# Kernel tuning notes

Measured on AMD Instinct MI355X. Metric: run time of the kernel, lower is better.

## Reference

```python
import jax, jax.numpy as jnp
import numpy as np

B, H, S, D = 2, 16, 2048, 64

def setup_inputs() -> dict:
    key = jax.random.key(0)
    kq, kk, kv = jax.random.split(key, 3)
    Q = jax.random.normal(kq, (B, H, S, D), dtype=jnp.float32)
    K = jax.random.normal(kk, (B, H, S, D), dtype=jnp.float32)
    V = jax.random.normal(kv, (B, H, S, D), dtype=jnp.float32)
    # causal mask, broadcastable over batch and heads
    mask = jnp.tril(jnp.ones((S, S), dtype=bool))[None, None, :, :]
    return {"Q": Q, "K": K, "V": V, "mask": mask}

def reference(Q, K, V, mask):
    # scores: [B,H,S,S]
    scores = jnp.einsum('bhqd,bhkd->bhqk', Q, K)
    # original applies mask (-inf) BEFORE scaling; -inf/scale == -inf so math matches
    scores = jnp.where(mask, scores, -jnp.inf)
    scores = scores / jnp.sqrt(jnp.float32(K.shape[-1]))
    attn = jax.nn.softmax(scores, axis=-1)
    return jnp.einsum('bhqk,bhkd->bhqd', attn, V)
```

## Files before the change

### kernel.cpp

```cpp
#include <hip/hip_runtime.h>

#define SEQ 2048
#define HD  64
#define SCALE 0.18033688011111772f

typedef __bf16 bf16x8 __attribute__((ext_vector_type(8)));
typedef __bf16 bf16x4 __attribute__((ext_vector_type(4)));
typedef float  f32x4  __attribute__((ext_vector_type(4)));
typedef float  f32x16 __attribute__((ext_vector_type(16)));

#define BAR_LGKM() asm volatile("s_waitcnt lgkmcnt(0)\n\ts_barrier" ::: "memory")

__global__ __launch_bounds__(256, 4) void attn_fwd(
    const float* __restrict__ Q,
    const float* __restrict__ K,
    const float* __restrict__ V,
    float* __restrict__ O)
{
    __shared__ __align__(16) unsigned char smem[26624];
    #define KBp(kh,key,c8) ((__bf16*)(smem +         (((kh)<<12) + ((key)<<7) + ((c8)<<4))))
    #define VTp(kh,r,c8)   ((__bf16*)(smem +  8192 + (((kh)<<12) + ((r)<<6)   + ((c8)<<4))))
    #define PWp(w,n,koff)  ((__bf16*)(smem + 16384 + ((w)*2560 + (n)*80 + ((koff)<<1))))

    const int tid   = threadIdx.x;
    const int wave  = tid >> 6;
    const int lane  = tid & 63;
    const int n     = lane & 31;
    const int p     = lane >> 5;
    const int strip = wave & 1;
    const int kh    = wave >> 1;

    const int x  = blockIdx.x;
    const int bh = x & 31;
    const int s  = x >> 5;
    const int q  = (s & 16) ? (31 - (s & 15)) : s;

    const int q0    = q * 64 + strip * 32;
    const int iters = q + 1;
    const int tS0   = kh * (q + 1);

    const float* __restrict__ Qh = Q + (size_t)bh * SEQ * HD;
    const float* __restrict__ Kh = K + (size_t)bh * SEQ * HD;
    const float* __restrict__ Vh = V + (size_t)bh * SEQ * HD;
    float* __restrict__       Oh = O + (size_t)bh * SEQ * HD;

    bf16x8 qf[4];
    {
        const float* qrow = Qh + (size_t)(q0 + n) * HD;
        #pragma unroll
        for (int c = 0; c < 4; ++c) {
            f32x4 a = *(const f32x4*)(qrow + 16 * c + 8 * p);
            f32x4 b = *(const f32x4*)(qrow + 16 * c + 8 * p + 4);
            #pragma unroll
            for (int j = 0; j < 4; ++j) {
                qf[c][j]     = (__bf16)(a[j] * SCALE);
                qf[c][4 + j] = (__bf16)(b[j] * SCALE);
            }
        }
    }

    f32x16 oT[2] = {};
    float  l_own = 0.f;

    const int local = tid & 127;
    const int key_s = local >> 2;
    const int dgi   = local & 3;
    const int Ls    = local & 31;
    const int ko    = local >> 5;
    const int swk   = key_s & 7;
    const int swv   = Ls & 3;

    const float* kbase = Kh + (size_t)key_s * HD + dgi * 16;
    const float* vbase = Vh + (size_t)(ko * 8) * HD + 2 * Ls;

    f32x4  kst[4];
    float2 vst[8];
    {
        const float* kp = kbase + (size_t)(32 * tS0) * HD;
        #pragma unroll
        for (int i = 0; i < 4; ++i) kst[i] = *(const f32x4*)(kp + 4 * i);
        const float* vp = vbase + (size_t)(32 * tS0) * HD;
        #pragma unroll
        for (int i = 0; i < 8; ++i) vst[i] = *(const float2*)(vp + (size_t)i * HD);
    }

    for (int i = 0; i < iters; ++i) {
        BAR_LGKM();

        {
            bf16x8 w0, w1;
            #pragma unroll
            for (int j = 0; j < 4; ++j) {
                w0[j] = (__bf16)kst[0][j]; w0[4 + j] = (__bf16)kst[1][j];
                w1[j] = (__bf16)kst[2][j]; w1[4 + j] = (__bf16)kst[3][j];
            }
            *(bf16x8*)KBp(kh, key_s, (2 * dgi)     ^ swk) = w0;
            *(bf16x8*)KBp(kh, key_s, (2 * dgi + 1) ^ swk) = w1;

            bf16x8 v0, v1;
            #pragma unroll
            for (int j = 0; j < 8; ++j) { v0[j] = (__bf16)vst[j].x; v1[j] = (__bf16)vst[j].y; }
            *(bf16x8*)VTp(kh, 2 * Ls,     ko ^ swv) = v0;
            *(bf16x8*)VTp(kh, 2 * Ls + 1, ko ^ swv) = v1;
        }

        if (i + 1 < iters) {
            const size_t off = (size_t)(32 * (tS0 + i + 1)) * HD;
            const float* kp = kbase + off;
            #pragma unroll
            for (int j = 0; j < 4; ++j) kst[j] = *(const f32x4*)(kp + 4 * j);
            const float* vp = vbase + off;
            #pragma unroll
            for (int j = 0; j < 8; ++j) vst[j] = *(const float2*)(vp + (size_t)j * HD);
        }

        BAR_LGKM();

        if (!kh || (i < q + strip)) {
            f32x16 sT = {};
            #pragma unroll
            for (int cc = 0; cc < 4; ++cc) {
                bf16x8 kf = *(const bf16x8*)KBp(kh, n, (2 * cc + p) ^ (n & 7));
                sT = __builtin_amdgcn_mfma_f32_32x32x16_bf16(kf, qf[cc], sT, 0, 0, 0);
            }

            const int  T    = tS0 + i;
            const bool diag = (T == 2 * q + strip);

            float pv[16];
            float ts = 0.f;
            #pragma unroll
            for (int r = 0; r < 16; ++r) {
                float pe = __builtin_amdgcn_exp2f(sT[r]);
                if (diag) {
                    const int kk = (r & 3) + 8 * (r >> 2) + 4 * p;
                    pe = (kk <= n) ? pe : 0.f;
                }
                pv[r] = pe;
                ts += pe;
            }
            l_own += ts;

            #pragma unroll
            for (int m = 0; m < 4; ++m) {
                bf16x4 pk;
                #pragma unroll
                for (int j = 0; j < 4; ++j) pk[j] = (__bf16)pv[4 * m + j];
                *(bf16x4*)PWp(wave, n, 8 * m + 4 * p) = pk;
            }
            bf16x8 pf0 = *(const bf16x8*)PWp(wave, n, 8 * p);
            bf16x8 pf1 = *(const bf16x8*)PWp(wave, n, 16 + 8 * p);

            const int swn = (n >> 1) & 3;
            #pragma unroll
            for (int dg = 0; dg < 2; ++dg) {
                bf16x8 vf0 = *(const bf16x8*)VTp(kh, 32 * dg + n, p ^ swn);
                bf16x8 vf1 = *(const bf16x8*)VTp(kh, 32 * dg + n, (2 + p) ^ swn);
                oT[dg] = __builtin_amdgcn_mfma_f32_32x32x16_bf16(vf0, pf0, oT[dg], 0, 0, 0);
                oT[dg] = __builtin_amdgcn_mfma_f32_32x32x16_bf16(vf1, pf1, oT[dg], 0, 0, 0);
            }
        }
    }

    __syncthreads();
    float* Os = (float*)smem;
    const int cb = strip * 2112;
    float l_part = l_own + __shfl_xor(l_own, 32, 64);

    if (kh == 1) {
        #pragma unroll
        for (int dg = 0; dg < 2; ++dg)
            #pragma unroll
            for (int r = 0; r < 16; ++r)
                Os[cb + (dg * 16 + r) * 64 + lane] = oT[dg][r];
        Os[cb + 2048 + lane] = l_part;
    }
    __syncthreads();
    if (kh == 0) {
        const float linv = 1.0f / (l_part + Os[cb + 2048 + lane]);
        #pragma unroll
        for (int dg = 0; dg < 2; ++dg) {
            #pragma unroll
            for (int u = 0; u < 4; ++u) {
                f32x4 o;
                #pragma unroll
                for (int j = 0; j < 4; ++j) {
                    const int r = 4 * u + j;
                    o[j] = (oT[dg][r] + Os[cb + (dg * 16 + r) * 64 + lane]) * linv;
                }
                *(f32x4*)&Oh[(size_t)(q0 + n) * HD + dg * 32 + u * 8 + 4 * p] = o;
            }
        }
    }
}

extern "C" void kernel_launch(void* const* d_in, const int* in_sizes, int n_in,
                              void* d_out, int out_size, void* d_ws, size_t ws_size,
                              hipStream_t stream) {
    const float* Q = (const float*)d_in[0];
    const float* K = (const float*)d_in[1];
    const float* V = (const float*)d_in[2];
    float* O = (float*)d_out;

    dim3 grid(1024);
    dim3 block(256);
    attn_fwd<<<grid, block, 0, stream>>>(Q, K, V, O);
}
```

Measured before the change: 136.4 us.

## Double-buffer K/V tiles, swap P via permlane32 instead of LDS, add setprio

K/V shared-memory tiles are now double-buffered, so each iteration needs one barrier instead of two. The next tile is staged into the alternate buffer after compute, and global loads run two tiles ahead. The P matrix transpose through shared memory is replaced by bf16 packing plus v_permlane32_swap register exchanges. s_setprio raises wave priority around the MFMA section. This cuts barrier and LDS round-trip costs, but grows LDS to 32KB and extends register live ranges.

```diff
diff --git a/kernel.cpp b/kernel.cpp
--- a/kernel.cpp
+++ b/kernel.cpp
@@ -5,11 +5,29 @@
 #define SCALE 0.18033688011111772f
 
 typedef __bf16 bf16x8 __attribute__((ext_vector_type(8)));
-typedef __bf16 bf16x4 __attribute__((ext_vector_type(4)));
+typedef __bf16 bf16x2 __attribute__((ext_vector_type(2)));
 typedef float  f32x4  __attribute__((ext_vector_type(4)));
 typedef float  f32x16 __attribute__((ext_vector_type(16)));
 
 #define BAR_LGKM() asm volatile("s_waitcnt lgkmcnt(0)\n\ts_barrier" ::: "memory")
+
+union PU { unsigned u[4]; bf16x8 v; };
+
+__device__ __forceinline__ unsigned pk2(float lo, float hi) {
+    union { unsigned u; bf16x2 v; } t;
+    t.v = bf16x2{(__bf16)lo, (__bf16)hi};
+    return t.u;
+}
+
+__device__ __forceinline__ void plswap(unsigned &x, unsigned &y) {
+#if __has_builtin(__builtin_amdgcn_permlane32_swap)
+    auto r = __builtin_amdgcn_permlane32_swap(x, y, false, false);
+    x = (unsigned)r[0];
+    y = (unsigned)r[1];
+#else
+    asm("v_permlane32_swap_b32 %0, %1" : "+v"(x), "+v"(y));
+#endif
+}
 
 __global__ __launch_bounds__(256, 4) void attn_fwd(
     const float* __restrict__ Q,
@@ -17,10 +35,9 @@
     const float* __restrict__ V,
     float* __restrict__ O)
 {
-    __shared__ __align__(16) unsigned char smem[26624];
-    #define KBp(kh,key,c8) ((__bf16*)(smem +         (((kh)<<12) + ((key)<<7) + ((c8)<<4))))
-    #define VTp(kh,r,c8)   ((__bf16*)(smem +  8192 + (((kh)<<12) + ((r)<<6)   + ((c8)<<4))))
-    #define PWp(w,n,koff)  ((__bf16*)(smem + 16384 + ((w)*2560 + (n)*80 + ((koff)<<1))))
+    __shared__ __align__(16) unsigned char smem[32768];
+    #define KBp(kh,b,key,c8) ((__bf16*)(smem +         (((kh)<<13) + ((b)<<12) + ((key)<<7) + ((c8)<<4))))
+    #define VTp(kh,b,r,c8)   ((__bf16*)(smem + 16384 + (((kh)<<13) + ((b)<<12) + ((r)<<6)   + ((c8)<<4))))
 
     const int tid   = threadIdx.x;
     const int wave  = tid >> 6;
@@ -75,52 +92,48 @@
 
     f32x4  kst[4];
     float2 vst[8];
-    {
-        const float* kp = kbase + (size_t)(32 * tS0) * HD;
-        #pragma unroll
-        for (int i = 0; i < 4; ++i) kst[i] = *(const f32x4*)(kp + 4 * i);
-        const float* vp = vbase + (size_t)(32 * tS0) * HD;
-        #pragma unroll
-        for (int i = 0; i < 8; ++i) vst[i] = *(const float2*)(vp + (size_t)i * HD);
-    }
+
+    auto loadt = [&](int t) {
+        const size_t off = (size_t)(32 * t) * HD;
+        const float* kp = kbase + off;
+        #pragma unroll
+        for (int j = 0; j < 4; ++j) kst[j] = *(const f32x4*)(kp + 4 * j);
+        const float* vp = vbase + off;
+        #pragma unroll
+        for (int j = 0; j < 8; ++j) vst[j] = *(const float2*)(vp + (size_t)j * HD);
+    };
+
+    auto stage = [&](int nb) {
+        bf16x8 w0, w1;
+        #pragma unroll
+        for (int j = 0; j < 4; ++j) {
+            w0[j] = (__bf16)kst[0][j]; w0[4 + j] = (__bf16)kst[1][j];
+            w1[j] = (__bf16)kst[2][j]; w1[4 + j] = (__bf16)kst[3][j];
+        }
+        *(bf16x8*)KBp(kh, nb, key_s, (2 * dgi)     ^ swk) = w0;
+        *(bf16x8*)KBp(kh, nb, key_s, (2 * dgi + 1) ^ swk) = w1;
+
+        bf16x8 v0, v1;
+        #pragma unroll
+        for (int j = 0; j < 8; ++j) { v0[j] = (__bf16)vst[j].x; v1[j] = (__bf16)vst[j].y; }
+        *(bf16x8*)VTp(kh, nb, 2 * Ls,     ko ^ swv) = v0;
+        *(bf16x8*)VTp(kh, nb, 2 * Ls + 1, ko ^ swv) = v1;
+    };
+
+    loadt(tS0);
+    stage(0);
+    if (iters > 1) loadt(tS0 + 1);
 
     for (int i = 0; i < iters; ++i) {
         BAR_LGKM();
-
-        {
-            bf16x8 w0, w1;
-            #pragma unroll
-            for (int j = 0; j < 4; ++j) {
-                w0[j] = (__bf16)kst[0][j]; w0[4 + j] = (__bf16)kst[1][j];
-                w1[j] = (__bf16)kst[2][j]; w1[4 + j] = (__bf16)kst[3][j];
-            }
-            *(bf16x8*)KBp(kh, key_s, (2 * dgi)     ^ swk) = w0;
-            *(bf16x8*)KBp(kh, key_s, (2 * dgi + 1) ^ swk) = w1;
-
-            bf16x8 v0, v1;
-            #pragma unroll
-            for (int j = 0; j < 8; ++j) { v0[j] = (__bf16)vst[j].x; v1[j] = (__bf16)vst[j].y; }
-            *(bf16x8*)VTp(kh, 2 * Ls,     ko ^ swv) = v0;
-            *(bf16x8*)VTp(kh, 2 * Ls + 1, ko ^ swv) = v1;
-        }
-
-        if (i + 1 < iters) {
-            const size_t off = (size_t)(32 * (tS0 + i + 1)) * HD;
-            const float* kp = kbase + off;
-            #pragma unroll
-            for (int j = 0; j < 4; ++j) kst[j] = *(const f32x4*)(kp + 4 * j);
-            const float* vp = vbase + off;
-            #pragma unroll
-            for (int j = 0; j < 8; ++j) vst[j] = *(const float2*)(vp + (size_t)j * HD);
-        }
-
-        BAR_LGKM();
+        const int cur = i & 1;
 
         if (!kh || (i < q + strip)) {
+            __builtin_amdgcn_s_setprio(1);
             f32x16 sT = {};
             #pragma unroll
             for (int cc = 0; cc < 4; ++cc) {
-                bf16x8 kf = *(const bf16x8*)KBp(kh, n, (2 * cc + p) ^ (n & 7));
+                bf16x8 kf = *(const bf16x8*)KBp(kh, cur, n, (2 * cc + p) ^ (n & 7));
                 sT = __builtin_amdgcn_mfma_f32_32x32x16_bf16(kf, qf[cc], sT, 0, 0, 0);
             }
 
@@ -141,25 +154,33 @@
             }
             l_own += ts;
 
-            #pragma unroll
-            for (int m = 0; m < 4; ++m) {
-                bf16x4 pk;
-                #pragma unroll
-                for (int j = 0; j < 4; ++j) pk[j] = (__bf16)pv[4 * m + j];
-                *(bf16x4*)PWp(wave, n, 8 * m + 4 * p) = pk;
-            }
-            bf16x8 pf0 = *(const bf16x8*)PWp(wave, n, 8 * p);
-            bf16x8 pf1 = *(const bf16x8*)PWp(wave, n, 16 + 8 * p);
+            unsigned a0 = pk2(pv[0],  pv[1]),  a1 = pk2(pv[2],  pv[3]);
+            unsigned a2 = pk2(pv[4],  pv[5]),  a3 = pk2(pv[6],  pv[7]);
+            unsigned b0 = pk2(pv[8],  pv[9]),  b1 = pk2(pv[10], pv[11]);
+            unsigned b2 = pk2(pv[12], pv[13]), b3 = pk2(pv[14], pv[15]);
+            plswap(a0, a2);
+            plswap(a1, a3);
+            plswap(b0, b2);
+            plswap(b1, b3);
+            PU pu0, pu1;
+            pu0.u[0] = a0; pu0.u[1] = a1; pu0.u[2] = a2; pu0.u[3] = a3;
+            pu1.u[0] = b0; pu1.u[1] = b1; pu1.u[2] = b2; pu1.u[3] = b3;
+            bf16x8 pf0 = pu0.v;
+            bf16x8 pf1 = pu1.v;
 
             const int swn = (n >> 1) & 3;
             #pragma unroll
             for (int dg = 0; dg < 2; ++dg) {
-                bf16x8 vf0 = *(const bf16x8*)VTp(kh, 32 * dg + n, p ^ swn);
-                bf16x8 vf1 = *(const bf16x8*)VTp(kh, 32 * dg + n, (2 + p) ^ swn);
+                bf16x8 vf0 = *(const bf16x8*)VTp(kh, cur, 32 * dg + n, p ^ swn);
+                bf16x8 vf1 = *(const bf16x8*)VTp(kh, cur, 32 * dg + n, (2 + p) ^ swn);
                 oT[dg] = __builtin_amdgcn_mfma_f32_32x32x16_bf16(vf0, pf0, oT[dg], 0, 0, 0);
                 oT[dg] = __builtin_amdgcn_mfma_f32_32x32x16_bf16(vf1, pf1, oT[dg], 0, 0, 0);
             }
-        }
+            __builtin_amdgcn_s_setprio(0);
+        }
+
+        if (i + 1 < iters) stage(cur ^ 1);
+        if (i + 2 < iters) loadt(tS0 + i + 2);
     }
 
     __syncthreads();
```

Measured after the change: 132.2 us. -3.1%, faster.
